# Optimization experiments

Measured on AMD Instinct MI355X. Metric: run time of the kernel, lower is better.

The kernel has to match this reference:

```python
import jax, jax.numpy as jnp
import numpy as np

T, H, I, E = 1024, 2048, 1408, 32
TOPK, N_GROUP, TOPK_GROUP = 6, 4, 2
ROUTED_SCALE = 2.5  # config.routed_scaling_factor


def setup_inputs() -> dict:
    key = jax.random.key(0)
    ks = jax.random.split(key, 9)
    s = 0.02
    return {
        "hidden_states": jax.random.normal(ks[0], (T, H), jnp.float32),
        "gate_w": jax.random.normal(ks[1], (E, H), jnp.float32) * s,   # router linear weight
        "e_bias": jax.random.normal(ks[2], (E,), jnp.float32) * s,     # e_score_correction_bias
        "w_gate": jax.random.normal(ks[3], (E, H, I), jnp.float32) * s,
        "w_up": jax.random.normal(ks[4], (E, H, I), jnp.float32) * s,
        "w_down": jax.random.normal(ks[5], (E, I, H), jnp.float32) * s,
        "sw_gate": jax.random.normal(ks[6], (H, I), jnp.float32) * s,  # shared expert
        "sw_up": jax.random.normal(ks[7], (H, I), jnp.float32) * s,
        "sw_down": jax.random.normal(ks[8], (I, H), jnp.float32) * s,
    }


def _grouped_topk(scores, e_bias):
    """DeepSeek-V3 'noaux_tc' grouped top-k: sigmoid scores, bias-corrected
    selection, group pruning via sum of per-group top-2, renormalized weights
    taken from the UNbiased scores."""
    sfc = scores + e_bias[None, :]                         # [T,E] scores_for_choice
    g = sfc.reshape(T, N_GROUP, E // N_GROUP)
    top2, _ = jax.lax.top_k(g, 2)
    group_scores = top2.sum(-1)                            # [T, n_group]
    _, gidx = jax.lax.top_k(group_scores, TOPK_GROUP)      # [T, topk_group]
    gmask = jax.nn.one_hot(gidx, N_GROUP, dtype=scores.dtype).sum(1)  # [T, n_group]
    emask = jnp.repeat(gmask, E // N_GROUP, axis=1)        # [T, E]
    masked = jnp.where(emask > 0, sfc, -jnp.inf)
    _, topk_ids = jax.lax.top_k(masked, TOPK)              # [T, topk]
    topk_w = jnp.take_along_axis(scores, topk_ids, axis=1) # gather unbiased scores
    topk_w = topk_w / (topk_w.sum(-1, keepdims=True) + 1e-20)  # renormalize=True
    return topk_w, topk_ids


def reference(hidden_states, gate_w, e_bias, w_gate, w_up, w_down, sw_gate, sw_up, sw_down):
    x = hidden_states  # [T,H]
    # shared expert SwiGLU MLP (gate_up_proj -> npu_swiglu -> down_proj)
    shared = (jax.nn.silu(x @ sw_gate) * (x @ sw_up)) @ sw_down  # [T,H]
    # router
    logits = x @ gate_w.T                                        # [T,E]
    scores = jax.nn.sigmoid(logits.astype(jnp.float32))
    topk_w, topk_ids = _grouped_topk(scores, e_bias)
    # FusedMoE: dispatch/grouped-GEMM/combine, expressed densely via a
    # scatter of top-k weights into a [T,E] combine matrix (zeros for
    # unselected experts), matching the fused kernel's math exactly.
    combine = jnp.zeros((T, E), x.dtype).at[jnp.arange(T)[:, None], topk_ids].add(
        topk_w.astype(x.dtype))
    g = jnp.einsum('th,ehi->tei', x, w_gate)   # [T,E,I]
    u = jnp.einsum('th,ehi->tei', x, w_up)
    h = jax.nn.silu(g) * u
    expert_out = jnp.einsum('tei,eih->teh', h, w_down)  # [T,E,H]
    routed = jnp.einsum('te,teh->th', combine, expert_out)
    return routed * ROUTED_SCALE + shared
```

## Files before the change

### kernel.cpp

```cpp
#include <hip/hip_runtime.h>
#include <cstdint>

#define T 1024
#define H 2048
#define II 1408
#define E 32
#define TOPK 6
#define NGRP 4
#define GSZ 8
#define CAP 1024
#define CAPH 384

typedef __attribute__((ext_vector_type(8))) short short8;
typedef __attribute__((ext_vector_type(4))) float f32x4;
typedef __attribute__((ext_vector_type(2))) unsigned int u32x2;
typedef __attribute__((ext_vector_type(4))) unsigned short us4;

static __device__ __forceinline__ unsigned short f2bf(float f) {
    unsigned int u = __builtin_bit_cast(unsigned int, f);
    u += 0x7FFFu + ((u >> 16) & 1u);
    return (unsigned short)(u >> 16);
}

static __device__ __forceinline__ unsigned int cvtpk(float lo, float hi) {
    unsigned int r;
    asm("v_cvt_pk_bf16_f32 %0, %1, %2" : "=v"(r) : "v"(lo), "v"(hi));
    return r;
}

#define KBAR() { \
        asm volatile("s_waitcnt lgkmcnt(0)" ::: "memory"); \
        __builtin_amdgcn_s_barrier(); \
        __builtin_amdgcn_sched_barrier(0); }

__global__ void prep_kernel(const float* __restrict__ x, unsigned short* __restrict__ xbf,
                            int* __restrict__ list, float* __restrict__ wts,
                            int* __restrict__ cnt) {
    int gid = blockIdx.x * blockDim.x + threadIdx.x;
    const int n4 = T * H / 4;
    if (gid < n4) {
        const float4 v = reinterpret_cast<const float4*>(x)[gid];
        us4 o;
        o.x = f2bf(v.x); o.y = f2bf(v.y); o.z = f2bf(v.z); o.w = f2bf(v.w);
        reinterpret_cast<us4*>(xbf)[gid] = o;
    }
    if (gid < T) { list[E * CAP + gid] = gid; wts[E * CAP + gid] = 1.0f; }
    if (gid < E + 1) cnt[gid] = (gid == E) ? T : 0;
}

__global__ __launch_bounds__(256) void router_kernel(
        const float* __restrict__ x, const float* __restrict__ gw,
        const float* __restrict__ bias, int* __restrict__ list,
        float* __restrict__ wts, int* __restrict__ cnt) {
    int t = blockIdx.x;
    int tid = threadIdx.x;
    int e = tid >> 3, p = tid & 7;
    const float4* xr = reinterpret_cast<const float4*>(x + (size_t)t * H);
    const float4* gr = reinterpret_cast<const float4*>(gw + (size_t)e * H);
    float part = 0.f;
    for (int q = 0; q < 64; ++q) {
        int idx = p * 64 + q;
        float4 a = xr[idx], b = gr[idx];
        part += a.x * b.x + a.y * b.y + a.z * b.z + a.w * b.w;
    }
    __shared__ float red[256];
    __shared__ float sc[E], sfc[E];
    red[tid] = part;
    __syncthreads();
    if (tid < E) {
        float s = 0.f;
        for (int j = 0; j < 8; ++j) s += red[tid * 8 + j];
        float sig = 1.f / (1.f + expf(-s));
        sc[tid] = sig;
        sfc[tid] = sig + bias[tid];
    }
    __syncthreads();
    if (tid == 0) {
        float gs[NGRP];
        for (int g = 0; g < NGRP; ++g) {
            float m1 = -INFINITY, m2 = -INFINITY;
            for (int j = 0; j < GSZ; ++j) {
                float v = sfc[g * GSZ + j];
                if (v > m1) { m2 = m1; m1 = v; }
                else if (v > m2) m2 = v;
            }
            gs[g] = m1 + m2;
        }
        int g1 = 0;
        for (int g = 1; g < NGRP; ++g) if (gs[g] > gs[g1]) g1 = g;
        int g2 = -1;
        for (int g = 0; g < NGRP; ++g) {
            if (g == g1) continue;
            if (g2 < 0 || gs[g] > gs[g2]) g2 = g;
        }
        int sel[TOPK];
        unsigned int usedmask = 0;
        float wsum = 0.f;
        for (int k = 0; k < TOPK; ++k) {
            float best = -INFINITY; int bi = -1;
            for (int ee = 0; ee < E; ++ee) {
                int g = ee >> 3;
                if (g != g1 && g != g2) continue;
                if (usedmask & (1u << ee)) continue;
                if (sfc[ee] > best) { best = sfc[ee]; bi = ee; }
            }
            usedmask |= (1u << bi);
            sel[k] = bi;
            wsum += sc[bi];
        }
        float fac = 2.5f / (wsum + 1e-20f);
        for (int k = 0; k < TOPK; ++k) {
            int ee = sel[k];
            int pos = atomicAdd(&cnt[ee], 1);
            list[ee * CAP + pos] = t;
            wts[ee * CAP + pos] = sc[ee] * fac;
        }
    }
}

__global__ __launch_bounds__(256, 2) void passA_kernel(
        const unsigned short* __restrict__ xbf,
        const float* __restrict__ wgate, const float* __restrict__ wup,
        const float* __restrict__ swgate, const float* __restrict__ swup,
        const int* __restrict__ list, const int* __restrict__ cnt,
        unsigned short* __restrict__ h) {
    int bx = blockIdx.x;
    int ve, start, end;
    if (bx < E) { ve = bx; start = 0; end = cnt[ve]; }
    else        { ve = E; start = (bx - E) * 256; end = start + 256; }
    if (start >= end) return;
    const int i0 = blockIdx.y * 32;
    const int tid = threadIdx.x, wave = tid >> 6, lane = tid & 63;
    const int lcol = lane & 15, lkg = lane >> 4;
    const int mat = tid >> 7;
    const int wcq = tid & 7;
    const int wkq = (tid >> 3) & 15;
    const float* G = (ve < E) ? wgate + (size_t)ve * H * II : swgate;
    const float* U = (ve < E) ? wup   + (size_t)ve * H * II : swup;
    const float* Wsrc = (mat ? U : G) + (size_t)(wkq * 4) * II + i0 + wcq * 4;
    __shared__ unsigned short lB[2][2][32 * 64];
    __shared__ int tokL[256];
    const int slotbase = (ve < E) ? ve * CAPH : E * CAPH;

#define LOADPF_A(PF, KS) { \
        const float* src = Wsrc + (size_t)((KS) * 64) * II; \
        _Pragma("unroll") \
        for (int q = 0; q < 4; ++q) \
            PF[q] = *reinterpret_cast<const f32x4*>(src + (size_t)q * II); }

#define AISS_A(AR, KS) { \
        _Pragma("unroll") \
        for (int s = 0; s < 2; ++s) \
            _Pragma("unroll") \
            for (int m = 0; m < 4; ++m) \
                AR[s][m] = *reinterpret_cast<const short8*>(&xrow[m][(KS) * 64 + s * 32 + lkg * 8]); }

#define STAGE_A(BUF, PF) { \
        char* dst = (char*)&lB[BUF][mat][0]; \
        _Pragma("unroll") \
        for (int c = 0; c < 4; ++c) { \
            int ii = wcq * 4 + c; \
            unsigned int ad = ((unsigned)ii * 128 + (unsigned)wkq * 8) ^ (((unsigned)(ii & 7)) << 4); \
            u32x2 pk; \
            pk[0] = cvtpk(PF[0][c], PF[1][c]); \
            pk[1] = cvtpk(PF[2][c], PF[3][c]); \
            *reinterpret_cast<u32x2*>(dst + ad) = pk; \
        } }

#define ITER_A(KS, CUR, ACUR, ANXT, PFISS, PFSTG) { \
        if (wact && (KS) + 1 < 32) AISS_A(ANXT, (KS) + 1) \
        __builtin_amdgcn_sched_barrier(0); \
        if ((KS) + 2 < 32) LOADPF_A(PFISS, (KS) + 2) \
        __builtin_amdgcn_sched_barrier(0); \
        if (wact) { \
            const char* b0 = (const char*)&lB[CUR][0][0]; \
            const char* b1 = (const char*)&lB[CUR][1][0]; \
            __builtin_amdgcn_s_setprio(1); \
            _Pragma("unroll") \
            for (int s = 0; s < 2; ++s) { \
                _Pragma("unroll") \
                for (int n = 0; n < 2; ++n) { \
                    unsigned int ra = ((unsigned)(n * 16 + lcol) * 128 + (unsigned)(s * 64 + lkg * 16)) \
                                    ^ (((unsigned)(lcol & 7)) << 4); \
                    const short8 bg = *reinterpret_cast<const short8*>(b0 + ra); \
                    const short8 bu = *reinterpret_cast<const short8*>(b1 + ra); \
                    _Pragma("unroll") \
                    for (int m = 0; m < 4; ++m) { \
                        accg[m][n] = __builtin_amdgcn_mfma_f32_16x16x32_bf16(ACUR[s][m], bg, accg[m][n], 0, 0, 0); \
                        accu[m][n] = __builtin_amdgcn_mfma_f32_16x16x32_bf16(ACUR[s][m], bu, accu[m][n], 0, 0, 0); \
                    } \
                } \
            } \
            __builtin_amdgcn_s_setprio(0); \
        } \
        if ((KS) + 1 < 32) STAGE_A((CUR) ^ 1, PFSTG) \
        KBAR() }

    for (int m0 = start; m0 < end; m0 += 256) {
        int msize = min(256, end - m0);
        tokL[tid] = (tid < msize) ? list[ve * CAP + m0 + tid] : 0;
        f32x4 accg[4][2] = {};
        f32x4 accu[4][2] = {};
        f32x4 pfA[4], pfB[4];
        short8 aA[2][4], aB[2][4];
        __syncthreads();
        const unsigned short* xrow[4];
        #pragma unroll
        for (int m = 0; m < 4; ++m)
            xrow[m] = xbf + (size_t)tokL[wave * 64 + m * 16 + lcol] * H;
        bool wact = (wave * 64) < msize;
        LOADPF_A(pfA, 0)
        if (wact) AISS_A(aA, 0)
        STAGE_A(0, pfA)
        LOADPF_A(pfB, 1)
        KBAR()

        #pragma unroll 1
        for (int ks = 0; ks < 32; ks += 2) {
            ITER_A(ks, 0, aA, aB, pfA, pfB)
            ITER_A(ks + 1, 1, aB, aA, pfB, pfA)
        }
        if (wact) {
            #pragma unroll
            for (int m = 0; m < 4; ++m)
                #pragma unroll
                for (int n = 0; n < 2; ++n)
                    #pragma unroll
                    for (int r = 0; r < 4; ++r) {
                        int rowl = wave * 64 + m * 16 + lkg * 4 + r;
                        int pos = m0 + rowl;
                        bool ok = (rowl < msize) && !(ve < E && pos >= CAPH);
                        float gv = accg[m][n][r], uv = accu[m][n][r];
                        float hv = gv / (1.f + expf(-gv)) * uv;
                        if (ok)
                            h[(size_t)(slotbase + pos) * II + i0 + n * 16 + lcol] = f2bf(hv);
                    }
        }
        __syncthreads();
    }
#undef ITER_A
#undef STAGE_A
#undef AISS_A
#undef LOADPF_A
}

__global__ __launch_bounds__(256, 2) void passB_kernel(
        const unsigned short* __restrict__ h,
        const float* __restrict__ wdown, const float* __restrict__ swdown,
        const int* __restrict__ list, const float* __restrict__ wts,
        const int* __restrict__ cnt, float* __restrict__ out) {
    int bx = blockIdx.x;
    int ve, start, end;
    if (bx < E) { ve = bx; start = 0; end = cnt[ve]; }
    else        { ve = E; start = (bx - E) * 256; end = start + 256; }
    if (start >= end) return;
    const float* W = (ve < E) ? wdown + (size_t)ve * II * H : swdown;
    const int n0 = blockIdx.y * 64;
    const int tid = threadIdx.x, wave = tid >> 6, lane = tid & 63;
    const int lcol = lane & 15, lkg = lane >> 4;
    const int wnq = tid & 15;
    const int wkq = tid >> 4;
    const float* Wsrc = W + (size_t)(wkq * 4) * H + n0 + wnq * 4;
    __shared__ unsigned short lW[2][64 * 64];
    __shared__ int tokL[256];
    __shared__ float wtL[256];
    const int slotbase = (ve < E) ? ve * CAPH : E * CAPH;
    const int NS = II / 64;

#define LOADPF_B(PF, KS) { \
        const float* src = Wsrc + (size_t)((KS) * 64) * H; \
        _Pragma("unroll") \
        for (int q = 0; q < 4; ++q) \
            PF[q] = *reinterpret_cast<const f32x4*>(src + (size_t)q * H); }

#define AISS_B(AR, KS) { \
        _Pragma("unroll") \
        for (int s = 0; s < 2; ++s) \
            _Pragma("unroll") \
            for (int m = 0; m < 4; ++m) \
                AR[s][m] = *reinterpret_cast<const short8*>(&hrow[m][(KS) * 64 + s * 32 + lkg * 8]); }

#define STAGE_B(BUF, PF) { \
        char* dst = (char*)&lW[BUF][0]; \
        _Pragma("unroll") \
        for (int c = 0; c < 4; ++c) { \
            int nn = wnq * 4 + c; \
            unsigned int ad = ((unsigned)nn * 128 + (unsigned)wkq * 8) ^ (((unsigned)(nn & 7)) << 4); \
            u32x2 pk; \
            pk[0] = cvtpk(PF[0][c], PF[1][c]); \
            pk[1] = cvtpk(PF[2][c], PF[3][c]); \
            *reinterpret_cast<u32x2*>(dst + ad) = pk; \
        } }

#define ITER_B(KS, CUR, ACUR, ANXT, PFISS, PFSTG) { \
        if (wact && (KS) + 1 < NS) AISS_B(ANXT, (KS) + 1) \
        __builtin_amdgcn_sched_barrier(0); \
        if ((KS) + 2 < NS) LOADPF_B(PFISS, (KS) + 2) \
        __builtin_amdgcn_sched_barrier(0); \
        if (wact) { \
            const char* bw0 = (const char*)&lW[CUR][0]; \
            __builtin_amdgcn_s_setprio(1); \
            _Pragma("unroll") \
            for (int s = 0; s < 2; ++s) { \
                _Pragma("unroll") \
                for (int n = 0; n < 4; ++n) { \
                    unsigned int ra = ((unsigned)(n * 16 + lcol) * 128 + (unsigned)(s * 64 + lkg * 16)) \
                                    ^ (((unsigned)(lcol & 7)) << 4); \
                    const short8 b = *reinterpret_cast<const short8*>(bw0 + ra); \
                    _Pragma("unroll") \
                    for (int m = 0; m < 4; ++m) \
                        acc[m][n] = __builtin_amdgcn_mfma_f32_16x16x32_bf16(ACUR[s][m], b, acc[m][n], 0, 0, 0); \
                } \
            } \
            __builtin_amdgcn_s_setprio(0); \
        } \
        if ((KS) + 1 < NS) STAGE_B((CUR) ^ 1, PFSTG) \
        KBAR() }

    for (int m0 = start; m0 < end; m0 += 256) {
        int msize = min(256, end - m0);
        tokL[tid] = (tid < msize) ? list[ve * CAP + m0 + tid] : 0;
        wtL[tid]  = (tid < msize) ? wts[ve * CAP + m0 + tid] : 0.f;
        f32x4 acc[4][4] = {};
        f32x4 pfA[4], pfB[4];
        short8 aA[2][4], aB[2][4];
        __syncthreads();
        const unsigned short* hrow[4];
        #pragma unroll
        for (int m = 0; m < 4; ++m)
            hrow[m] = h + (size_t)(slotbase + m0 + wave * 64 + m * 16 + lcol) * II;
        bool wact = (wave * 64) < msize;
        LOADPF_B(pfA, 0)
        if (wact) AISS_B(aA, 0)
        STAGE_B(0, pfA)
        LOADPF_B(pfB, 1)
        KBAR()

        #pragma unroll 1
        for (int ks = 0; ks < NS; ks += 2) {
            ITER_B(ks, 0, aA, aB, pfA, pfB)
            ITER_B(ks + 1, 1, aB, aA, pfB, pfA)
        }
        if (wact) {
            #pragma unroll
            for (int m = 0; m < 4; ++m)
                #pragma unroll
                for (int n = 0; n < 4; ++n)
                    #pragma unroll
                    for (int r = 0; r < 4; ++r) {
                        int rowl = wave * 64 + m * 16 + lkg * 4 + r;
                        if (rowl < msize) {
                            int tok = tokL[rowl];
                            float wv = wtL[rowl];
                            unsafeAtomicAdd(&out[(size_t)tok * H + n0 + n * 16 + lcol],
                                            acc[m][n][r] * wv);
                        }
                    }
        }
        __syncthreads();
    }
#undef ITER_B
#undef STAGE_B
#undef AISS_B
#undef LOADPF_B
}

extern "C" void kernel_launch(void* const* d_in, const int* in_sizes, int n_in,
                              void* d_out, int out_size, void* d_ws, size_t ws_size,
                              hipStream_t stream) {
    const float* x       = (const float*)d_in[0];
    const float* gate_w  = (const float*)d_in[1];
    const float* e_bias  = (const float*)d_in[2];
    const float* w_gate  = (const float*)d_in[3];
    const float* w_up    = (const float*)d_in[4];
    const float* w_down  = (const float*)d_in[5];
    const float* sw_gate = (const float*)d_in[6];
    const float* sw_up   = (const float*)d_in[7];
    const float* sw_down = (const float*)d_in[8];
    float* out = (float*)d_out;

    char* ws = (char*)d_ws;
    unsigned short* xbf = (unsigned short*)ws;
    int*   list = (int*)(ws + 4194304);
    float* wts  = (float*)(ws + 4194304 + 135168);
    int*   cnt  = (int*)(ws + 4194304 + 2 * 135168);
    unsigned short* h = (unsigned short*)(ws + 4194304 + 2 * 135168 + 256);

    hipMemsetAsync(d_out, 0, (size_t)T * H * sizeof(float), stream);
    prep_kernel<<<dim3(2048), dim3(256), 0, stream>>>(x, xbf, list, wts, cnt);
    router_kernel<<<dim3(T), dim3(256), 0, stream>>>(x, gate_w, e_bias, list, wts, cnt);
    passA_kernel<<<dim3(36, 44), dim3(256), 0, stream>>>(xbf, w_gate, w_up, sw_gate, sw_up, list, cnt, h);
    passB_kernel<<<dim3(36, 32), dim3(256), 0, stream>>>(h, w_down, sw_down, list, wts, cnt, out);
}
```

Baseline: 504.6 us.

## Widen passA column tile to 64 and simplify prefetch/A-fragment pipeline

New measurement: 595.2 us. +18.0%, slower.

```diff
diff --git a/kernel.cpp b/kernel.cpp
--- a/kernel.cpp
+++ b/kernel.cpp
@@ -14,6 +14,7 @@
 typedef __attribute__((ext_vector_type(8))) short short8;
 typedef __attribute__((ext_vector_type(4))) float f32x4;
 typedef __attribute__((ext_vector_type(2))) unsigned int u32x2;
+typedef __attribute__((ext_vector_type(4))) unsigned int u32x4;
 typedef __attribute__((ext_vector_type(4))) unsigned short us4;
 
 static __device__ __forceinline__ unsigned short f2bf(float f) {
@@ -129,23 +130,24 @@
     if (bx < E) { ve = bx; start = 0; end = cnt[ve]; }
     else        { ve = E; start = (bx - E) * 256; end = start + 256; }
     if (start >= end) return;
-    const int i0 = blockIdx.y * 32;
+    const int i0 = blockIdx.y * 64;
     const int tid = threadIdx.x, wave = tid >> 6, lane = tid & 63;
     const int lcol = lane & 15, lkg = lane >> 4;
     const int mat = tid >> 7;
-    const int wcq = tid & 7;
-    const int wkq = (tid >> 3) & 15;
+    const int sub = tid & 127;
+    const int wiq = sub & 15;
+    const int wkq = sub >> 4;
     const float* G = (ve < E) ? wgate + (size_t)ve * H * II : swgate;
     const float* U = (ve < E) ? wup   + (size_t)ve * H * II : swup;
-    const float* Wsrc = (mat ? U : G) + (size_t)(wkq * 4) * II + i0 + wcq * 4;
-    __shared__ unsigned short lB[2][2][32 * 64];
+    const float* Wsrc = (mat ? U : G) + (size_t)(wkq * 8) * II + i0 + wiq * 4;
+    __shared__ unsigned short lB[2][2][64 * 64];
     __shared__ int tokL[256];
     const int slotbase = (ve < E) ? ve * CAPH : E * CAPH;
 
 #define LOADPF_A(PF, KS) { \
         const float* src = Wsrc + (size_t)((KS) * 64) * II; \
         _Pragma("unroll") \
-        for (int q = 0; q < 4; ++q) \
+        for (int q = 0; q < 8; ++q) \
             PF[q] = *reinterpret_cast<const f32x4*>(src + (size_t)q * II); }
 
 #define AISS_A(AR, KS) { \
@@ -159,18 +161,21 @@
         char* dst = (char*)&lB[BUF][mat][0]; \
         _Pragma("unroll") \
         for (int c = 0; c < 4; ++c) { \
-            int ii = wcq * 4 + c; \
-            unsigned int ad = ((unsigned)ii * 128 + (unsigned)wkq * 8) ^ (((unsigned)(ii & 7)) << 4); \
-            u32x2 pk; \
+            int ii = wiq * 4 + c; \
+            unsigned int ad = ((unsigned)ii * 128 + (unsigned)wkq * 16) ^ (((unsigned)(ii & 7)) << 4); \
+            u32x4 pk; \
             pk[0] = cvtpk(PF[0][c], PF[1][c]); \
             pk[1] = cvtpk(PF[2][c], PF[3][c]); \
-            *reinterpret_cast<u32x2*>(dst + ad) = pk; \
+            pk[2] = cvtpk(PF[4][c], PF[5][c]); \
+            pk[3] = cvtpk(PF[6][c], PF[7][c]); \
+            *reinterpret_cast<u32x4*>(dst + ad) = pk; \
         } }
 
-#define ITER_A(KS, CUR, ACUR, ANXT, PFISS, PFSTG) { \
-        if (wact && (KS) + 1 < 32) AISS_A(ANXT, (KS) + 1) \
+#define ITER_A(KS, CUR) { \
+        short8 a[2][4]; \
+        if (wact) AISS_A(a, KS) \
         __builtin_amdgcn_sched_barrier(0); \
-        if ((KS) + 2 < 32) LOADPF_A(PFISS, (KS) + 2) \
+        if ((KS) + 1 < 32) LOADPF_A(pf, (KS) + 1) \
         __builtin_amdgcn_sched_barrier(0); \
         if (wact) { \
             const char* b0 = (const char*)&lB[CUR][0][0]; \
@@ -179,52 +184,49 @@
             _Pragma("unroll") \
             for (int s = 0; s < 2; ++s) { \
                 _Pragma("unroll") \
-                for (int n = 0; n < 2; ++n) { \
+                for (int n = 0; n < 4; ++n) { \
                     unsigned int ra = ((unsigned)(n * 16 + lcol) * 128 + (unsigned)(s * 64 + lkg * 16)) \
                                     ^ (((unsigned)(lcol & 7)) << 4); \
                     const short8 bg = *reinterpret_cast<const short8*>(b0 + ra); \
                     const short8 bu = *reinterpret_cast<const short8*>(b1 + ra); \
                     _Pragma("unroll") \
                     for (int m = 0; m < 4; ++m) { \
-                        accg[m][n] = __builtin_amdgcn_mfma_f32_16x16x32_bf16(ACUR[s][m], bg, accg[m][n], 0, 0, 0); \
-                        accu[m][n] = __builtin_amdgcn_mfma_f32_16x16x32_bf16(ACUR[s][m], bu, accu[m][n], 0, 0, 0); \
+                        accg[m][n] = __builtin_amdgcn_mfma_f32_16x16x32_bf16(a[s][m], bg, accg[m][n], 0, 0, 0); \
+                        accu[m][n] = __builtin_amdgcn_mfma_f32_16x16x32_bf16(a[s][m], bu, accu[m][n], 0, 0, 0); \
                     } \
                 } \
             } \
             __builtin_amdgcn_s_setprio(0); \
         } \
-        if ((KS) + 1 < 32) STAGE_A((CUR) ^ 1, PFSTG) \
+        if ((KS) + 1 < 32) STAGE_A((CUR) ^ 1, pf) \
         KBAR() }
 
     for (int m0 = start; m0 < end; m0 += 256) {
         int msize = min(256, end - m0);
         tokL[tid] = (tid < msize) ? list[ve * CAP + m0 + tid] : 0;
-        f32x4 accg[4][2] = {};
-        f32x4 accu[4][2] = {};
-        f32x4 pfA[4], pfB[4];
-        short8 aA[2][4], aB[2][4];
+        f32x4 accg[4][4] = {};
+        f32x4 accu[4][4] = {};
+        f32x4 pf[8];
         __syncthreads();
         const unsigned short* xrow[4];
         #pragma unroll
         for (int m = 0; m < 4; ++m)
             xrow[m] = xbf + (size_t)tokL[wave * 64 + m * 16 + lcol] * H;
         bool wact = (wave * 64) < msize;
-        LOADPF_A(pfA, 0)
-        if (wact) AISS_A(aA, 0)
-        STAGE_A(0, pfA)
-        LOADPF_A(pfB, 1)
+        LOADPF_A(pf, 0)
+        STAGE_A(0, pf)
         KBAR()
 
         #pragma unroll 1
         for (int ks = 0; ks < 32; ks += 2) {
-            ITER_A(ks, 0, aA, aB, pfA, pfB)
-            ITER_A(ks + 1, 1, aB, aA, pfB, pfA)
+            ITER_A(ks, 0)
+            ITER_A(ks + 1, 1)
         }
         if (wact) {
             #pragma unroll
             for (int m = 0; m < 4; ++m)
                 #pragma unroll
-                for (int n = 0; n < 2; ++n)
+                for (int n = 0; n < 4; ++n)
                     #pragma unroll
                     for (int r = 0; r < 4; ++r) {
                         int rowl = wave * 64 + m * 16 + lkg * 4 + r;
@@ -389,6 +391,6 @@
     hipMemsetAsync(d_out, 0, (size_t)T * H * sizeof(float), stream);
     prep_kernel<<<dim3(2048), dim3(256), 0, stream>>>(x, xbf, list, wts, cnt);
     router_kernel<<<dim3(T), dim3(256), 0, stream>>>(x, gate_w, e_bias, list, wts, cnt);
-    passA_kernel<<<dim3(36, 44), dim3(256), 0, stream>>>(xbf, w_gate, w_up, sw_gate, sw_up, list, cnt, h);
+    passA_kernel<<<dim3(36, 22), dim3(256), 0, stream>>>(xbf, w_gate, w_up, sw_gate, sw_up, list, cnt, h);
     passB_kernel<<<dim3(36, 32), dim3(256), 0, stream>>>(h, w_down, sw_down, list, wts, cnt, out);
 }
```
